# Kernel optimization log

Measured on AMD Instinct MI355X. Metric: run time of the kernel, lower is better.

Reference implementation:

```python
import jax, jax.numpy as jnp
import numpy as np

DIM = 256
NUM_HEADS = 8
NUM_NEI = (16, 32)
G = len(NUM_NEI)          # branches
G_H = NUM_HEADS // G      # heads per branch = 4
G_DIM = DIM // G          # channels per branch = 128
HD = G_DIM // G_H         # head dim = 32
SCALE = HD ** (-0.5)
M_MSF = G                 # MSF branches
CHANNEL = DIM // M_MSF    # 128
D_MSF = CHANNEL           # r=1

gelu = lambda t: jax.nn.gelu(t, approximate=False)


def setup_inputs() -> dict:
    key = jax.random.key(0)
    ks = jax.random.split(key, 16)
    B, N = 4, 2048
    s = lambda fan: fan ** (-0.5)
    inp = {
        "x": jax.random.normal(ks[0], (B, N, DIM), jnp.float32),
        "pos": jax.random.uniform(ks[1], (B, N, 3), jnp.float32),
        # qkv linear (no bias); stored as (in, out)
        "Wqkv": jax.random.normal(ks[2], (DIM, 3 * DIM), jnp.float32) * s(DIM),
        # per-branch rel-pos MLPs: Linear(3, g_dim) + GELU
        "Wp0": jax.random.normal(ks[3], (3, G_DIM), jnp.float32) * s(3),
        "bp0": jnp.zeros((G_DIM,), jnp.float32),
        "Wp1": jax.random.normal(ks[4], (3, G_DIM), jnp.float32) * s(3),
        "bp1": jnp.zeros((G_DIM,), jnp.float32),
        # MSF params
        "W_proj": jax.random.normal(ks[5], (DIM, DIM), jnp.float32) * s(DIM),
        "b_proj": jnp.zeros((DIM,), jnp.float32),
        "W_fc1": jax.random.normal(ks[6], (DIM, D_MSF), jnp.float32) * s(DIM),
        "b_fc1": jnp.zeros((D_MSF,), jnp.float32),
        "W_fc2": jax.random.normal(ks[7], (D_MSF, M_MSF * CHANNEL), jnp.float32) * s(D_MSF),
        "b_fc2": jnp.zeros((M_MSF * CHANNEL,), jnp.float32),
        "W_head": jax.random.normal(ks[8], (DIM, DIM), jnp.float32) * s(DIM),
        "b_head": jnp.zeros((DIM,), jnp.float32),
    }
    return inp


def _branch(q, k, v, pos, knn_idx, Wp, bp):
    """One head-group: KNN gather + rel-pos MLP fused attention.
    q,k,v: [B,N,g_dim]; pos: [B,N,3]; knn_idx: [B,N,nk]."""
    B, N, g_dim = k.shape
    nk = knn_idx.shape[-1]
    gather = jax.vmap(lambda t, idx: t[idx])  # per-batch fancy gather -> [B,N,nk,D]
    knn_xyz = gather(pos, knn_idx)                       # [B,N,nk,3]
    kg = gather(k, knn_idx)                              # [B,N,nk,g_dim]
    vg = gather(v, knn_idx)
    # split heads: b n k (h d) -> b h n k d
    split = lambda t: t.reshape(B, N, nk, G_H, HD).transpose(0, 3, 1, 2, 4)
    kg, vg = split(kg), split(vg)
    rel = pos[:, :, None, :] - knn_xyz                   # [B,N,nk,3]
    vrp = split(gelu(rel @ Wp + bp))                     # [B,h,N,nk,d]
    vg = vg + vrp
    attn_rel = vrp.sum(-1)                               # [B,h,N,nk]
    qh = q.reshape(B, N, G_H, HD).transpose(0, 2, 1, 3)  # [B,h,N,d]
    logits = jnp.einsum('bhnd,bhnkd->bhnk', qh, kg) * SCALE + attn_rel
    a = jax.nn.softmax(logits, axis=-1)
    out = jnp.einsum('bhnk,bhnkd->bhnd', a, vg)          # [B,h,N,d]
    return out.transpose(0, 2, 1, 3).reshape(B, N, g_dim)


def _msf(x, W_proj, b_proj, W_fc1, b_fc1, W_fc2, b_fc2, W_head, b_head):
    bs, N, dim = x.shape
    input_groups = x.transpose(0, 2, 1).reshape(bs, M_MSF, CHANNEL, N)
    feats_proj = gelu(x @ W_proj + b_proj)               # [bs,N,dim]
    feats_S = feats_proj.mean(axis=1)                    # global avg pool over N -> [bs,dim]
    feats_Z = gelu(feats_S @ W_fc1 + b_fc1)
    av = (feats_Z @ W_fc2 + b_fc2).reshape(bs, M_MSF, CHANNEL, 1)
    av = jax.nn.softmax(av, axis=1)                      # softmax over branches
    feats_V = (input_groups * av).reshape(bs, dim, N).transpose(0, 2, 1)
    feats_V = feats_V @ W_head + b_head
    return feats_proj + feats_V


def reference(x, pos, Wqkv, Wp0, bp0, Wp1, bp1,
              W_proj, b_proj, W_fc1, b_fc1, W_fc2, b_fc2, W_head, b_head):
    B, N, C = x.shape
    # pairwise squared distances [B,N,N] (broadcast form, as in source)
    dists = jnp.sum((pos[:, :, None, :] - pos[:, None, :, :]) ** 2, axis=-1)
    order = jnp.argsort(dists, axis=-1)                  # [B,N,N]
    qkv = (x @ Wqkv).reshape(B, N, 3, C).transpose(2, 0, 1, 3)  # [3,B,N,C]
    pos_params = [(Wp0, bp0), (Wp1, bp1)]
    outs = []
    for i, nk in enumerate(NUM_NEI):
        sl = slice(i * G_DIM, (i + 1) * G_DIM)
        q, k, v = qkv[0][..., sl], qkv[1][..., sl], qkv[2][..., sl]
        knn_idx = order[:, :, :nk]
        Wp, bp = pos_params[i]
        outs.append(_branch(q, k, v, pos, knn_idx, Wp, bp))
    xcat = jnp.concatenate(outs, axis=-1)                # [B,N,C]
    return _msf(xcat, W_proj, b_proj, W_fc1, b_fc1, W_fc2, b_fc2, W_head, b_head)
```

## Files before the change

### kernel.cpp

```cpp
#include <hip/hip_runtime.h>
#include <cstdint>
#include <cstddef>

#define B_    4
#define NPT   2048
#define DIM_  256
#define QKVW  768
#define XLEN  2097152
#define QLEN  196608
#define PLEN  65536
#define TOTC  (XLEN + QLEN + 2 * PLEN)

typedef unsigned short ushort_t;
typedef unsigned long long u64;
typedef short bf16x8 __attribute__((ext_vector_type(8)));
typedef float f32x4 __attribute__((ext_vector_type(4)));

__device__ __forceinline__ float gelu_f(float x) {
  return 0.5f * x * (1.0f + erff(x * 0.70710678118654752440f));
}

__device__ __forceinline__ float gelu_fast(float x) {
  const float is2 = 0.70710678118654752440f;
  float z = x * is2;
  float az = __builtin_fabsf(z);
  float t = __builtin_amdgcn_rcpf(fmaf(0.3275911f, az, 1.0f));
  float p = fmaf(1.061405429f, t, -1.453152027f);
  p = fmaf(p, t, 1.421413741f);
  p = fmaf(p, t, -0.284496736f);
  p = fmaf(p, t, 0.254829592f);
  p = p * t;
  float e = __expf(-az * az);
  float er = fmaf(-p, e, 1.0f);
  er = __builtin_copysignf(er, x);
  return 0.5f * x * (1.0f + er);
}

__device__ __forceinline__ ushort_t f2bf(float f) {
  unsigned u = __float_as_uint(f);
  unsigned r = (u + 0x7fffu + ((u >> 16) & 1u)) >> 16;
  return (ushort_t)r;
}
__device__ __forceinline__ float bf2f(ushort_t h) {
  return __uint_as_float(((unsigned)h) << 16);
}

template <int CTRL>
__device__ __forceinline__ void dppmin_step(int& lo, int& hi) {
  int olo = __builtin_amdgcn_update_dpp(lo, lo, CTRL, 0xf, 0xf, false);
  int ohi = __builtin_amdgcn_update_dpp(hi, hi, CTRL, 0xf, 0xf, false);
  u64 o = ((u64)(unsigned)ohi << 32) | (unsigned)olo;
  u64 c = ((u64)(unsigned)hi << 32) | (unsigned)lo;
  if (o < c) { lo = olo; hi = ohi; }
}
template <int CTRL>
__device__ __forceinline__ float dpp_addf(float x) {
  int s = __builtin_amdgcn_update_dpp(0, __float_as_int(x), CTRL, 0xf, 0xf, false);
  return x + __int_as_float(s);
}
template <int CTRL>
__device__ __forceinline__ int dpp_addi(int x) {
  int s = __builtin_amdgcn_update_dpp(0, x, CTRL, 0xf, 0xf, false);
  return x + s;
}
__device__ __forceinline__ float head32_reduce(float u) {
  u = dpp_addf<0x111>(u);
  u = dpp_addf<0x112>(u);
  u = dpp_addf<0x114>(u);
  u = dpp_addf<0x118>(u);
  u = dpp_addf<0x142>(u);
  return u;
}
__device__ __forceinline__ int wave_sum_i(int x) {
  x = dpp_addi<0x111>(x);
  x = dpp_addi<0x112>(x);
  x = dpp_addi<0x114>(x);
  x = dpp_addi<0x118>(x);
  x = dpp_addi<0x142>(x);
  x = dpp_addi<0x143>(x);
  return x;
}
__device__ __forceinline__ u64 wave_min64(u64 k) {
  int lo = (int)(unsigned)(k & 0xffffffffULL);
  int hi = (int)(unsigned)(k >> 32);
  dppmin_step<0x111>(lo, hi);
  dppmin_step<0x112>(lo, hi);
  dppmin_step<0x114>(lo, hi);
  dppmin_step<0x118>(lo, hi);
  dppmin_step<0x142>(lo, hi);
  dppmin_step<0x143>(lo, hi);
  unsigned glo = (unsigned)__builtin_amdgcn_readlane(lo, 63);
  unsigned ghi = (unsigned)__builtin_amdgcn_readlane(hi, 63);
  return ((u64)ghi << 32) | glo;
}

__device__ __forceinline__ bf16x8 scale_bf(bf16x8 v, const float* avk) {
  bf16x8 r;
#pragma unroll
  for (int e = 0; e < 8; e++) {
    float f = bf2f((ushort_t)v[e]) * avk[e];
    r[e] = (short)f2bf(f);
  }
  return r;
}

__global__ __launch_bounds__(256) void prep_kernel(
    const float* __restrict__ pos, const float* __restrict__ x,
    const float* __restrict__ Wqkv, const float* __restrict__ Wproj,
    const float* __restrict__ Whead, int* __restrict__ idx_out,
    ushort_t* __restrict__ xbf, ushort_t* __restrict__ WqkvT,
    ushort_t* __restrict__ WprojT, ushort_t* __restrict__ WheadT,
    float* __restrict__ part) {
  int tid = threadIdx.x;
  if (blockIdx.x >= 2048) {
    int base = (blockIdx.x - 2048) * 256 + tid;
    if (base < 1024) part[base] = 0.f;
    for (int i = base; i < TOTC; i += 2048 * 256) {
      if (i < XLEN) {
        xbf[i] = f2bf(x[i]);
      } else if (i < XLEN + QLEN) {
        int e = i - XLEN;
        int k = e / 768, n = e - k * 768;
        WqkvT[n * 256 + k] = f2bf(Wqkv[e]);
      } else if (i < XLEN + QLEN + PLEN) {
        int e = i - XLEN - QLEN;
        int k = e >> 8, n = e & 255;
        WprojT[n * 256 + k] = f2bf(Wproj[e]);
      } else {
        int e = i - XLEN - QLEN - PLEN;
        int k = e >> 8, n = e & 255;
        WheadT[n * 256 + k] = f2bf(Whead[e]);
      }
    }
    return;
  }
  __shared__ u64 buf[4][128];
  __shared__ unsigned cnt[4];
  int wave = tid >> 6, lane = tid & 63;
  int wq = blockIdx.x * 4 + wave;
  int b = wq >> 11, n = wq & (NPT - 1);
  const float* pb = pos + (size_t)b * NPT * 3;
  float qx = pb[n * 3 + 0], qy = pb[n * 3 + 1], qz = pb[n * 3 + 2];
  u64 keys[32];
  {
#pragma clang fp contract(off)
#pragma unroll
    for (int s = 0; s < 32; s++) {
      int j = lane + (s << 6);
      float dx = qx - pb[j * 3 + 0];
      float dy = qy - pb[j * 3 + 1];
      float dz = qz - pb[j * 3 + 2];
      float d = dx * dx;
      d = d + dy * dy;
      d = d + dz * dz;
      keys[s] = ((u64)__float_as_uint(d) << 32) | (unsigned)j;
    }
  }
  unsigned lo = 0, hi = 0x40400001u;
  for (int it = 0; it < 31 && hi - lo > 1; ++it) {
    unsigned mid = (lo + hi) >> 1;
    int c = 0;
#pragma unroll
    for (int s = 0; s < 32; s++)
      c += ((unsigned)(keys[s] >> 32) < mid) ? 1 : 0;
    c = __builtin_amdgcn_readlane(wave_sum_i(c), 63);
    if (c >= 32) { hi = mid; if (c <= 64) break; }
    else lo = mid;
  }
  unsigned T = hi;
  buf[wave][lane] = ~0ULL;
  buf[wave][lane + 64] = ~0ULL;
  if (lane == 0) cnt[wave] = 0;
  __builtin_amdgcn_wave_barrier();
  asm volatile("s_waitcnt lgkmcnt(0)" ::: "memory");
  int cl = 0;
#pragma unroll
  for (int s = 0; s < 32; s++)
    cl += ((unsigned)(keys[s] >> 32) < T) ? 1 : 0;
  unsigned base = atomicAdd(&cnt[wave], (unsigned)cl);
  unsigned w = base;
#pragma unroll
  for (int s = 0; s < 32; s++) {
    if ((unsigned)(keys[s] >> 32) < T && w < 128) {
      buf[wave][w] = keys[s];
      w++;
    }
  }
  __builtin_amdgcn_wave_barrier();
  asm volatile("s_waitcnt lgkmcnt(0)" ::: "memory");
  u64 k0 = buf[wave][lane];
  u64 k1 = buf[wave][lane + 64];
  __builtin_amdgcn_wave_barrier();
  asm volatile("s_waitcnt lgkmcnt(0)" ::: "memory");
  int keep = 0;
  u64 lkey = (k0 < k1) ? k0 : k1;
  for (int r = 0; r < 32; r++) {
    u64 g = wave_min64(lkey);
    if (lane == r) keep = (int)(unsigned)(g & 0xffffffffULL);
    if (k0 == g) k0 = ~0ULL;
    if (k1 == g) k1 = ~0ULL;
    lkey = (k0 < k1) ? k0 : k1;
  }
  if (lane < 32) idx_out[(size_t)wq * 32 + lane] = keep;
}

template <int MODE>
__global__ __launch_bounds__(64, 4) void gemm_rf(
    const ushort_t* __restrict__ A, const ushort_t* __restrict__ BT,
    const float* __restrict__ bias, const float* __restrict__ extra,
    float* __restrict__ C, float* __restrict__ part,
    const float* __restrict__ av, int N) {
  constexpr int K = 256;
  int lane = threadIdx.x;
  int quad = lane >> 4, r16 = lane & 15;
  int t0 = blockIdx.x;
  int m0, n0;
  if (MODE == 0) { m0 = (t0 / 24) * 64; n0 = (t0 % 24) * 32; }
  else           { m0 = (t0 >> 3) * 64; n0 = (t0 & 7) * 32; }
  int batch = m0 >> 11;
  const ushort_t* Ap = A + (size_t)(m0 + r16) * K + quad * 8;
  const ushort_t* Bp = BT + (size_t)(n0 + r16) * K + quad * 8;
  f32x4 acc[4][2] = {};
  bf16x8 af[4], bf[2], af2[4], bf2[2];
#pragma unroll
  for (int i = 0; i < 4; i++) af[i] = *(const bf16x8*)(Ap + (size_t)i * 16 * K);
#pragma unroll
  for (int j = 0; j < 2; j++) bf[j] = *(const bf16x8*)(Bp + (size_t)j * 16 * K);
#pragma unroll
  for (int kc = 0; kc < 8; kc++) {
    if (kc < 7) {
      int ko = (kc + 1) * 32;
#pragma unroll
      for (int i = 0; i < 4; i++)
        af2[i] = *(const bf16x8*)(Ap + (size_t)i * 16 * K + ko);
#pragma unroll
      for (int j = 0; j < 2; j++)
        bf2[j] = *(const bf16x8*)(Bp + (size_t)j * 16 * K + ko);
    }
    bf16x8 b0 = bf[0], b1 = bf[1];
    if (MODE == 2) {
      const float* avk = av + batch * 256 + kc * 32 + quad * 8;
      b0 = scale_bf(b0, avk);
      b1 = scale_bf(b1, avk);
    }
#pragma unroll
    for (int i = 0; i < 4; i++) {
      acc[i][0] = __builtin_amdgcn_mfma_f32_16x16x32_bf16(af[i], b0, acc[i][0], 0, 0, 0);
      acc[i][1] = __builtin_amdgcn_mfma_f32_16x16x32_bf16(af[i], b1, acc[i][1], 0, 0, 0);
    }
#pragma unroll
    for (int i = 0; i < 4; i++) af[i] = af2[i];
    bf[0] = bf2[0]; bf[1] = bf2[1];
  }
  float cs[2] = {};
#pragma unroll
  for (int i = 0; i < 4; i++) {
#pragma unroll
    for (int j = 0; j < 2; j++) {
      int col = n0 + j * 16 + r16;
#pragma unroll
      for (int r = 0; r < 4; r++) {
        int row = m0 + i * 16 + quad * 4 + r;
        float v = acc[i][j][r];
        if (MODE == 1) { v = gelu_fast(v + bias[col]); cs[j] += v; }
        else if (MODE == 2) v = extra[(size_t)row * 256 + col] + v + bias[col];
        C[(size_t)row * N + col] = v;
      }
    }
  }
  if (MODE == 1) {
#pragma unroll
    for (int j = 0; j < 2; j++) {
      cs[j] += __shfl_xor(cs[j], 16, 64);
      cs[j] += __shfl_xor(cs[j], 32, 64);
    }
    if (quad == 0) {
#pragma unroll
      for (int j = 0; j < 2; j++)
        atomicAdd(&part[batch * 256 + n0 + j * 16 + r16], cs[j]);
    }
  }
}

template <int NK>
__device__ __forceinline__ float attn_loop(
    const float* __restrict__ qkvb, const int* sidx, const float4* srel,
    int g, int c, int lane, float qS, float w0, float w1, float w2, float bb) {
  float den = 0.f, num = 0.f;
#pragma unroll
  for (int j = 0; j < NK; j++) {
    int jj = __builtin_amdgcn_readfirstlane(sidx[j]);
    float4 rr = srel[j];
    const float* kb = qkvb + (size_t)jj * QKVW + 256 + g * 128;
    float kv = kb[c];
    float vv = kb[256 + c];
    float x = fmaf(rr.x, w0, fmaf(rr.y, w1, fmaf(rr.z, w2, bb)));
    float x2 = x * x;
    float z2 = x * fmaf(0.0713548163f, x2, 1.5957691216f);
    float t = __builtin_amdgcn_rcpf(1.0f + __expf(-z2));
    float r = x * t;
    float u = head32_reduce(fmaf(qS, kv, r));
    float l0 = __int_as_float(__builtin_amdgcn_readlane(__float_as_int(u), 31));
    float l1 = __int_as_float(__builtin_amdgcn_readlane(__float_as_int(u), 63));
    float logit = (lane < 32) ? l0 : l1;
    float e = __expf(logit);
    den += e;
    num = fmaf(e, vv + r, num);
  }
  return num * __builtin_amdgcn_rcpf(den);
}

__global__ __launch_bounds__(128) void attn_kernel(
    const float* __restrict__ qkv, const float* __restrict__ pos,
    const int* __restrict__ knn,
    const float* __restrict__ Wp0, const float* __restrict__ bp0,
    const float* __restrict__ Wp1, const float* __restrict__ bp1,
    ushort_t* __restrict__ xcat) {
  const float SCALE = 0.17677669529663687f;
  int u = blockIdx.x;
  int g = blockIdx.y;
  int b = u >> 11, n = u & (NPT - 1);
  int c = threadIdx.x;
  int wave = c >> 6, lane = c & 63;
  __shared__ int s_idx[2][32];
  __shared__ float4 s_rel[2][32];
  const float* qkvb = qkv + (size_t)b * NPT * QKVW;
  if (lane < 32) {
    int j = knn[(size_t)u * 32 + lane];
    s_idx[wave][lane] = j;
    const float* pn = pos + ((size_t)b * NPT + n) * 3;
    const float* pj = pos + ((size_t)b * NPT + j) * 3;
    s_rel[wave][lane] = make_float4(pn[0] - pj[0], pn[1] - pj[1],
                                    pn[2] - pj[2], 0.f);
  }
  __builtin_amdgcn_wave_barrier();
  asm volatile("s_waitcnt lgkmcnt(0)" ::: "memory");
  const float* Wp = g ? Wp1 : Wp0;
  const float* bp = g ? bp1 : bp0;
  float w0 = Wp[c], w1 = Wp[128 + c], w2 = Wp[256 + c], bb = bp[c];
  float qS = qkvb[(size_t)n * QKVW + g * 128 + c] * SCALE;
  float o = (g == 0)
      ? attn_loop<16>(qkvb, s_idx[wave], s_rel[wave], g, c, lane, qS, w0, w1, w2, bb)
      : attn_loop<32>(qkvb, s_idx[wave], s_rel[wave], g, c, lane, qS, w0, w1, w2, bb);
  xcat[((size_t)b * NPT + n) * DIM_ + g * 128 + c] = f2bf(o);
}

__global__ __launch_bounds__(256) void msf_av_kernel(
    const float* __restrict__ part, const float* __restrict__ Wfc1,
    const float* __restrict__ bfc1, const float* __restrict__ Wfc2,
    const float* __restrict__ bfc2, float* __restrict__ av_out) {
  int b = blockIdx.x, t = threadIdx.x;
  __shared__ float S[256], Z[128], A[256];
  S[t] = part[b * 256 + t] * (1.0f / 2048.0f);
  __syncthreads();
  if (t < 128) {
    float z = bfc1[t];
    for (int i = 0; i < 256; i++) z += S[i] * Wfc1[i * 128 + t];
    Z[t] = gelu_f(z);
  }
  __syncthreads();
  float a = bfc2[t];
  for (int j = 0; j < 128; j++) a += Z[j] * Wfc2[j * 256 + t];
  A[t] = a;
  __syncthreads();
  float pA = A[t ^ 128];
  float m = fmaxf(a, pA);
  float e = expf(a - m);
  av_out[b * 256 + t] = e / (e + expf(pA - m));
}

extern "C" void kernel_launch(void* const* d_in, const int* in_sizes, int n_in,
                              void* d_out, int out_size, void* d_ws, size_t ws_size,
                              hipStream_t stream) {
  const float* x     = (const float*)d_in[0];
  const float* pos   = (const float*)d_in[1];
  const float* Wqkv  = (const float*)d_in[2];
  const float* Wp0   = (const float*)d_in[3];
  const float* bp0   = (const float*)d_in[4];
  const float* Wp1   = (const float*)d_in[5];
  const float* bp1   = (const float*)d_in[6];
  const float* Wproj = (const float*)d_in[7];
  const float* bproj = (const float*)d_in[8];
  const float* Wfc1  = (const float*)d_in[9];
  const float* bfc1  = (const float*)d_in[10];
  const float* Wfc2  = (const float*)d_in[11];
  const float* bfc2  = (const float*)d_in[12];
  const float* Whead = (const float*)d_in[13];
  const float* bhead = (const float*)d_in[14];
  float* out = (float*)d_out;

  char* ws = (char*)d_ws;
  size_t off = 0;
  int* idx = (int*)(ws + off);              off += (size_t)B_ * NPT * 32 * 4;
  float* qkv = (float*)(ws + off);          off += (size_t)B_ * NPT * QKVW * 4;
  float* fp = qkv;
  ushort_t* xbf = (ushort_t*)(ws + off);    off += (size_t)B_ * NPT * DIM_ * 2;
  ushort_t* xcat = xbf;
  ushort_t* WqkvT = (ushort_t*)(ws + off);  off += (size_t)QLEN * 2;
  ushort_t* WprojT = (ushort_t*)(ws + off); off += (size_t)PLEN * 2;
  ushort_t* WheadT = (ushort_t*)(ws + off); off += (size_t)PLEN * 2;
  float* part = (float*)(ws + off);         off += 1024 * 4;
  float* av = (float*)(ws + off);           off += 1024 * 4;

  const int M = B_ * NPT;

  prep_kernel<<<4096, 256, 0, stream>>>(pos, x, Wqkv, Wproj, Whead,
                                        idx, xbf, WqkvT, WprojT, WheadT, part);
  gemm_rf<0><<<3072, 64, 0, stream>>>(xbf, WqkvT, nullptr, nullptr,
                                      qkv, nullptr, nullptr, QKVW);
  attn_kernel<<<dim3(M, 2), 128, 0, stream>>>(qkv, pos, idx,
                                              Wp0, bp0, Wp1, bp1, xcat);
  gemm_rf<1><<<1024, 64, 0, stream>>>(xcat, WprojT, bproj, nullptr,
                                      fp, part, nullptr, DIM_);
  msf_av_kernel<<<B_, 256, 0, stream>>>(part, Wfc1, bfc1, Wfc2, bfc2, av);
  gemm_rf<2><<<1024, 64, 0, stream>>>(xcat, WheadT, bhead, fp,
                                      out, nullptr, av, DIM_);
}
```

Before: 220.9 us.

## Replace serial KNN min-extraction with rank counting and co-schedule KNN with QKV GEMM

The top-32 selection no longer runs 32 serial wave-wide 64-bit DPP min reductions. Each lane now computes the rank of its candidate keys by comparing them against every key in the LDS buffer, then writes each key with rank below 32 straight to its slot. The KNN work also moves out of the conversion kernel into a combined launch with the QKV GEMM, as 64-thread blocks, so the two independent workloads can overlap. The bf16 conversion runs first as its own kernel. The cost is O(candidates) LDS reads per lane instead of 32 reduction rounds, plus a launch-order dependency change.

```diff
diff --git a/kernel.cpp b/kernel.cpp
--- a/kernel.cpp
+++ b/kernel.cpp
@@ -46,14 +46,6 @@
 }
 
 template <int CTRL>
-__device__ __forceinline__ void dppmin_step(int& lo, int& hi) {
-  int olo = __builtin_amdgcn_update_dpp(lo, lo, CTRL, 0xf, 0xf, false);
-  int ohi = __builtin_amdgcn_update_dpp(hi, hi, CTRL, 0xf, 0xf, false);
-  u64 o = ((u64)(unsigned)ohi << 32) | (unsigned)olo;
-  u64 c = ((u64)(unsigned)hi << 32) | (unsigned)lo;
-  if (o < c) { lo = olo; hi = ohi; }
-}
-template <int CTRL>
 __device__ __forceinline__ float dpp_addf(float x) {
   int s = __builtin_amdgcn_update_dpp(0, __float_as_int(x), CTRL, 0xf, 0xf, false);
   return x + __int_as_float(s);
@@ -80,19 +72,6 @@
   x = dpp_addi<0x143>(x);
   return x;
 }
-__device__ __forceinline__ u64 wave_min64(u64 k) {
-  int lo = (int)(unsigned)(k & 0xffffffffULL);
-  int hi = (int)(unsigned)(k >> 32);
-  dppmin_step<0x111>(lo, hi);
-  dppmin_step<0x112>(lo, hi);
-  dppmin_step<0x114>(lo, hi);
-  dppmin_step<0x118>(lo, hi);
-  dppmin_step<0x142>(lo, hi);
-  dppmin_step<0x143>(lo, hi);
-  unsigned glo = (unsigned)__builtin_amdgcn_readlane(lo, 63);
-  unsigned ghi = (unsigned)__builtin_amdgcn_readlane(hi, 63);
-  return ((u64)ghi << 32) | glo;
-}
 
 __device__ __forceinline__ bf16x8 scale_bf(bf16x8 v, const float* avk) {
   bf16x8 r;
@@ -104,40 +83,89 @@
   return r;
 }
 
-__global__ __launch_bounds__(256) void prep_kernel(
-    const float* __restrict__ pos, const float* __restrict__ x,
-    const float* __restrict__ Wqkv, const float* __restrict__ Wproj,
-    const float* __restrict__ Whead, int* __restrict__ idx_out,
+__global__ __launch_bounds__(256) void convert_kernel(
+    const float* __restrict__ x, const float* __restrict__ Wqkv,
+    const float* __restrict__ Wproj, const float* __restrict__ Whead,
     ushort_t* __restrict__ xbf, ushort_t* __restrict__ WqkvT,
     ushort_t* __restrict__ WprojT, ushort_t* __restrict__ WheadT,
     float* __restrict__ part) {
-  int tid = threadIdx.x;
-  if (blockIdx.x >= 2048) {
-    int base = (blockIdx.x - 2048) * 256 + tid;
-    if (base < 1024) part[base] = 0.f;
-    for (int i = base; i < TOTC; i += 2048 * 256) {
-      if (i < XLEN) {
-        xbf[i] = f2bf(x[i]);
-      } else if (i < XLEN + QLEN) {
-        int e = i - XLEN;
-        int k = e / 768, n = e - k * 768;
-        WqkvT[n * 256 + k] = f2bf(Wqkv[e]);
-      } else if (i < XLEN + QLEN + PLEN) {
-        int e = i - XLEN - QLEN;
-        int k = e >> 8, n = e & 255;
-        WprojT[n * 256 + k] = f2bf(Wproj[e]);
-      } else {
-        int e = i - XLEN - QLEN - PLEN;
-        int k = e >> 8, n = e & 255;
-        WheadT[n * 256 + k] = f2bf(Whead[e]);
+  int base = blockIdx.x * 256 + threadIdx.x;
+  if (base < 1024) part[base] = 0.f;
+  for (int i = base; i < TOTC; i += 2048 * 256) {
+    if (i < XLEN) {
+      xbf[i] = f2bf(x[i]);
+    } else if (i < XLEN + QLEN) {
+      int e = i - XLEN;
+      int k = e / 768, n = e - k * 768;
+      WqkvT[n * 256 + k] = f2bf(Wqkv[e]);
+    } else if (i < XLEN + QLEN + PLEN) {
+      int e = i - XLEN - QLEN;
+      int k = e >> 8, n = e & 255;
+      WprojT[n * 256 + k] = f2bf(Wproj[e]);
+    } else {
+      int e = i - XLEN - QLEN - PLEN;
+      int k = e >> 8, n = e & 255;
+      WheadT[n * 256 + k] = f2bf(Whead[e]);
+    }
+  }
+}
+
+__global__ __launch_bounds__(64, 4) void knn_gemm0_kernel(
+    const float* __restrict__ pos, int* __restrict__ idx_out,
+    const ushort_t* __restrict__ A, const ushort_t* __restrict__ BT,
+    float* __restrict__ C) {
+  __shared__ u64 buf[128];
+  __shared__ unsigned cnt;
+  int lane = threadIdx.x;
+  if (blockIdx.x >= 8192) {
+    constexpr int K = 256;
+    constexpr int N = 768;
+    int quad = lane >> 4, r16 = lane & 15;
+    int t0 = blockIdx.x - 8192;
+    int m0 = (t0 / 24) * 64, n0 = (t0 % 24) * 32;
+    const ushort_t* Ap = A + (size_t)(m0 + r16) * K + quad * 8;
+    const ushort_t* Bp = BT + (size_t)(n0 + r16) * K + quad * 8;
+    f32x4 acc[4][2] = {};
+    bf16x8 af[4], bfv[2], af2[4], bf2[2];
+#pragma unroll
+    for (int i = 0; i < 4; i++) af[i] = *(const bf16x8*)(Ap + (size_t)i * 16 * K);
+#pragma unroll
+    for (int j = 0; j < 2; j++) bfv[j] = *(const bf16x8*)(Bp + (size_t)j * 16 * K);
+#pragma unroll
+    for (int kc = 0; kc < 8; kc++) {
+      if (kc < 7) {
+        int ko = (kc + 1) * 32;
+#pragma unroll
+        for (int i = 0; i < 4; i++)
+          af2[i] = *(const bf16x8*)(Ap + (size_t)i * 16 * K + ko);
+#pragma unroll
+        for (int j = 0; j < 2; j++)
+          bf2[j] = *(const bf16x8*)(Bp + (size_t)j * 16 * K + ko);
       }
+#pragma unroll
+      for (int i = 0; i < 4; i++) {
+        acc[i][0] = __builtin_amdgcn_mfma_f32_16x16x32_bf16(af[i], bfv[0], acc[i][0], 0, 0, 0);
+        acc[i][1] = __builtin_amdgcn_mfma_f32_16x16x32_bf16(af[i], bfv[1], acc[i][1], 0, 0, 0);
+      }
+#pragma unroll
+      for (int i = 0; i < 4; i++) af[i] = af2[i];
+      bfv[0] = bf2[0]; bfv[1] = bf2[1];
+    }
+#pragma unroll
+    for (int i = 0; i < 4; i++) {
+#pragma unroll
+      for (int j = 0; j < 2; j++) {
+        int col = n0 + j * 16 + r16;
+#pragma unroll
+        for (int r = 0; r < 4; r++) {
+          int row = m0 + i * 16 + quad * 4 + r;
+          C[(size_t)row * N + col] = acc[i][j][r];
+        }
+      }
     }
     return;
   }
-  __shared__ u64 buf[4][128];
-  __shared__ unsigned cnt[4];
-  int wave = tid >> 6, lane = tid & 63;
-  int wq = blockIdx.x * 4 + wave;
+  int wq = blockIdx.x;
   int b = wq >> 11, n = wq & (NPT - 1);
   const float* pb = pos + (size_t)b * NPT * 3;
   float qx = pb[n * 3 + 0], qy = pb[n * 3 + 1], qz = pb[n * 3 + 2];
@@ -168,40 +196,43 @@
     else lo = mid;
   }
   unsigned T = hi;
-  buf[wave][lane] = ~0ULL;
-  buf[wave][lane + 64] = ~0ULL;
-  if (lane == 0) cnt[wave] = 0;
+  buf[lane] = ~0ULL;
+  buf[lane + 64] = ~0ULL;
+  if (lane == 0) cnt = 0;
   __builtin_amdgcn_wave_barrier();
   asm volatile("s_waitcnt lgkmcnt(0)" ::: "memory");
   int cl = 0;
 #pragma unroll
   for (int s = 0; s < 32; s++)
     cl += ((unsigned)(keys[s] >> 32) < T) ? 1 : 0;
-  unsigned base = atomicAdd(&cnt[wave], (unsigned)cl);
+  unsigned base = atomicAdd(&cnt, (unsigned)cl);
   unsigned w = base;
 #pragma unroll
   for (int s = 0; s < 32; s++) {
     if ((unsigned)(keys[s] >> 32) < T && w < 128) {
-      buf[wave][w] = keys[s];
+      buf[w] = keys[s];
       w++;
     }
   }
   __builtin_amdgcn_wave_barrier();
   asm volatile("s_waitcnt lgkmcnt(0)" ::: "memory");
-  u64 k0 = buf[wave][lane];
-  u64 k1 = buf[wave][lane + 64];
-  __builtin_amdgcn_wave_barrier();
-  asm volatile("s_waitcnt lgkmcnt(0)" ::: "memory");
-  int keep = 0;
-  u64 lkey = (k0 < k1) ? k0 : k1;
-  for (int r = 0; r < 32; r++) {
-    u64 g = wave_min64(lkey);
-    if (lane == r) keep = (int)(unsigned)(g & 0xffffffffULL);
-    if (k0 == g) k0 = ~0ULL;
-    if (k1 == g) k1 = ~0ULL;
-    lkey = (k0 < k1) ? k0 : k1;
-  }
-  if (lane < 32) idx_out[(size_t)wq * 32 + lane] = keep;
+  unsigned total = cnt;
+  total = (unsigned)__builtin_amdgcn_readfirstlane((int)total);
+  if (total > 128u) total = 128u;
+  unsigned mt = (total + 7u) & ~7u;
+  u64 k0 = buf[lane];
+  u64 k1 = buf[lane + 64];
+  int r0 = 0, r1 = 0;
+  for (unsigned i = 0; i < mt; i += 8) {
+#pragma unroll
+    for (int t = 0; t < 8; t++) {
+      u64 ki = buf[i + t];
+      r0 += (ki < k0) ? 1 : 0;
+      r1 += (ki < k1) ? 1 : 0;
+    }
+  }
+  if (r0 < 32) idx_out[(size_t)wq * 32 + r0] = (int)(unsigned)(k0 & 0xffffffffULL);
+  if (r1 < 32) idx_out[(size_t)wq * 32 + r1] = (int)(unsigned)(k1 & 0xffffffffULL);
 }
 
 template <int MODE>
@@ -214,9 +245,7 @@
   int lane = threadIdx.x;
   int quad = lane >> 4, r16 = lane & 15;
   int t0 = blockIdx.x;
-  int m0, n0;
-  if (MODE == 0) { m0 = (t0 / 24) * 64; n0 = (t0 % 24) * 32; }
-  else           { m0 = (t0 >> 3) * 64; n0 = (t0 & 7) * 32; }
+  int m0 = (t0 >> 3) * 64, n0 = (t0 & 7) * 32;
   int batch = m0 >> 11;
   const ushort_t* Ap = A + (size_t)(m0 + r16) * K + quad * 8;
   const ushort_t* Bp = BT + (size_t)(n0 + r16) * K + quad * 8;
@@ -404,10 +433,9 @@
 
   const int M = B_ * NPT;
 
-  prep_kernel<<<4096, 256, 0, stream>>>(pos, x, Wqkv, Wproj, Whead,
-                                        idx, xbf, WqkvT, WprojT, WheadT, part);
-  gemm_rf<0><<<3072, 64, 0, stream>>>(xbf, WqkvT, nullptr, nullptr,
-                                      qkv, nullptr, nullptr, QKVW);
+  convert_kernel<<<2048, 256, 0, stream>>>(x, Wqkv, Wproj, Whead,
+                                           xbf, WqkvT, WprojT, WheadT, part);
+  knn_gemm0_kernel<<<8192 + 3072, 64, 0, stream>>>(pos, idx, xbf, WqkvT, qkv);
   attn_kernel<<<dim3(M, 2), 128, 0, stream>>>(qkv, pos, idx,
                                               Wp0, bp0, Wp1, bp1, xcat);
   gemm_rf<1><<<1024, 64, 0, stream>>>(xcat, WprojT, bproj, nullptr,
```

Measured after the change: 203.2 us. -8.0%, faster.
